# Performance work log

Hardware: AMD Instinct MI355X
Metric: run time of the kernel (lower is better)

## Reference

```python
import jax, jax.numpy as jnp
import numpy as np

# SLAYER neuron / simulation parameters (from netParams)
THETA = 10.0      # spike threshold
TAU_SR = 10.0     # synaptic (psp) alpha-kernel time constant
TAU_REF = 1.0     # refractory alpha-kernel time constant
SCALE_REF = 2.0   # refractory kernel scale
TS = 1.0          # simulation time step

N, C, H, W_SP, T = 8, 2, 50, 63, 500
OUT = 128


def _alpha_scan(x_t_first, tau, gain):
    """Causal convolution with alpha kernel k[dt] = gain*(dt*TS/tau)*exp(1-dt*TS/tau),
    k[0]=0, expressed as an exact 2-state linear recursion (O(T) instead of O(T^2)).
    x_t_first: [T, ...]. Returns [T, ...]."""
    r = jnp.exp(jnp.asarray(-TS / tau, x_t_first.dtype))
    c = jnp.asarray(gain * (TS / tau) * np.e, x_t_first.dtype)

    def step(carry, xt):
        A, B = carry          # A = sum c*dt*r^dt, B = sum c*r^dt over past inputs
        out = A               # kernel is 0 at dt=0, so x[t] does not contribute yet
        Bp = B + c * xt
        return (r * (A + Bp), r * Bp), out

    zeros = jnp.zeros_like(x_t_first[0])
    _, out = jax.lax.scan(step, (zeros, zeros), x_t_first)
    return out


def _spike_scan(u_t_first):
    """SLAYER getSpikes: sequential threshold with refractory alpha kernel
    nu[dt] = -SCALE_REF*THETA*(dt*TS/TAU_REF)*exp(1-dt*TS/TAU_REF).
    u_t_first: [T, N, O] membrane input. Returns spikes [T, N, O]."""
    r = jnp.exp(jnp.asarray(-TS / TAU_REF, u_t_first.dtype))
    c = jnp.asarray(-SCALE_REF * THETA * (TS / TAU_REF) * np.e, u_t_first.dtype)

    def step(carry, ut):
        A, B = carry
        u = ut + A                       # membrane + accumulated refractory response
        s = (u >= THETA).astype(u.dtype)
        Bp = B + c * s
        return (r * (A + Bp), r * Bp), s

    zeros = jnp.zeros_like(u_t_first[0])
    _, s = jax.lax.scan(step, (zeros, zeros), u_t_first)
    return s


def setup_inputs() -> dict:
    key = jax.random.key(0)
    k1, k2 = jax.random.split(key)
    downsampled = (jax.random.uniform(k1, (N, C, H, W_SP, T)) < 0.05).astype(jnp.float32)
    W = jax.random.normal(k2, (OUT, C * H * W_SP), dtype=jnp.float32) * 0.05
    return {"downsampled": downsampled, "W": W}


def reference(downsampled, W):
    # psp: alpha-kernel temporal filter over every input element
    x = jnp.moveaxis(downsampled, -1, 0)            # [T, N, C, H, W]
    a = _alpha_scan(x, TAU_SR, 1.0)                  # [T, N, C, H, W]
    # dense: full-spatial projection per time step
    a = a.reshape(T, N, C * H * W_SP)                # [T, N, CHW]
    u = jnp.einsum('tnc,oc->tno', a, W)              # [T, N, OUT]
    # spike generation with refractory dynamics
    s = _spike_scan(u)                               # [T, N, OUT]
    s = jnp.moveaxis(s, 0, -1)                       # [N, OUT, T]
    return s.reshape(N, OUT, 1, 1, T)                # SLAYER dense output layout
```

## Files before the change

### kernel.cpp

```cpp
#include <hip/hip_runtime.h>

#define NB 8
#define CHW 6300
#define TT 500
#define OUT 128
#define NO 1024
#define NK32 200
#define KSPLIT 8
#define NKC (NK32/KSPLIT)

typedef __attribute__((ext_vector_type(8))) _Float16 f16x8;
typedef __attribute__((ext_vector_type(4))) float f32x4;

__global__ __launch_bounds__(512) void packW(const float* __restrict__ W,
                                             _Float16* __restrict__ Wp) {
    const int tid = threadIdx.x;
    const int osub = tid >> 6;
    const int lane = tid & 63;
    const int k32 = blockIdx.x;
    const int hl = blockIdx.y;
    const int o = osub * 16 + (lane & 15);
    const int cb = k32 * 32 + (lane >> 4) * 8;

    union { _Float16 h[8]; uint4 u; } tmp;
#pragma unroll
    for (int i = 0; i < 8; i++) {
        int c = cb + i;
        float w = (c < CHW) ? W[(size_t)o * CHW + c] : 0.f;
        _Float16 hi = (_Float16)w;
        tmp.h[i] = (hl == 0) ? hi : (_Float16)((w - (float)hi) * 2048.f);
    }
    size_t lr = (((size_t)hl * NK32 + k32) * 8 + osub) * 64 + lane;
    *(uint4*)(Wp + lr * 8) = tmp.u;
}

__global__ __launch_bounds__(256, 3) void gemm(const float* __restrict__ x,
                                               const _Float16* __restrict__ Wp,
                                               float* __restrict__ vp) {
    const int L = blockIdx.x;
    const int logical = (L & 7) * 64 + (L >> 3);
    const int tb = logical & 7;
    const int n  = (logical >> 3) & 7;
    const int ks = logical >> 6;

    const int tid = threadIdx.x;
    const int wave = tid >> 6;
    const int lane = tid & 63;
    const int l15 = lane & 15;
    const int lg  = lane >> 4;
    const int k32_0 = ks * NKC;

    __shared__ _Float16 Bs[2][4][512];

    const int t_st = tb * 64 + wave * 16 + l15;
    const bool t_ok = (t_st < TT);
    const float* xrow = x + (size_t)n * CHW * TT + t_st;

    f32x4 acc[2][4][2] = {};
    f16x8 Ar0[2][2], Ar1[2][2];
    float xvA[8], xvB[8];

#define XLOAD(xv, it)                                                              \
    {                                                                              \
        const int cb_ = (k32_0 + (it)) * 32 + lg * 8;                              \
        if (((k32_0 + (it) + 1) * 32 <= CHW) && t_ok) {                            \
            _Pragma("unroll") for (int i = 0; i < 8; i++)                          \
                xv[i] = xrow[(size_t)(cb_ + i) * TT];                              \
        } else {                                                                   \
            _Pragma("unroll") for (int i = 0; i < 8; i++)                          \
                xv[i] = (t_ok && (cb_ + i) < CHW) ? xrow[(size_t)(cb_ + i) * TT]   \
                                                  : 0.f;                           \
        }                                                                          \
    }

#define XWRITE(xv, buf)                                                            \
    {                                                                              \
        union { _Float16 h[8]; uint4 u; } tw_;                                     \
        _Pragma("unroll") for (int i = 0; i < 8; i++) tw_.h[i] = (_Float16)xv[i];  \
        *(uint4*)&Bs[buf][wave][lane * 8] = tw_.u;                                 \
    }

#define ALOAD(Ar, it)                                                              \
    _Pragma("unroll") for (int of = 0; of < 2; of++)                               \
        _Pragma("unroll") for (int hl = 0; hl < 2; hl++)                           \
            Ar[of][hl] = *(const f16x8*)(Wp +                                      \
                ((((size_t)hl * NK32 + k32_0 + (it)) * 8 + wave * 2 + of) * 64 +   \
                 lane) * 8);

#define COMPUTE(buf, Ar)                                                           \
    {                                                                              \
        f16x8 bfr[4];                                                              \
        _Pragma("unroll") for (int tf = 0; tf < 4; tf++)                           \
            bfr[tf] = *(const f16x8*)&Bs[buf][tf][lane * 8];                       \
        _Pragma("unroll") for (int of = 0; of < 2; of++)                           \
            _Pragma("unroll") for (int tf = 0; tf < 4; tf++)                       \
                _Pragma("unroll") for (int hl = 0; hl < 2; hl++)                   \
                    acc[of][tf][hl] = __builtin_amdgcn_mfma_f32_16x16x32_f16(      \
                        Ar[of][hl], bfr[tf], acc[of][tf][hl], 0, 0, 0);            \
    }

    XLOAD(xvA, 0)
    XLOAD(xvB, 1)
    ALOAD(Ar0, 0)
    XWRITE(xvA, 0)
    ALOAD(Ar1, 1)
    __syncthreads();

    for (int p = 0; p < 12; ++p) {
        const int it = 2 * p;
        XLOAD(xvA, it + 2)
        COMPUTE(0, Ar0)
        XWRITE(xvB, 1)
        ALOAD(Ar0, it + 2)
        __syncthreads();
        if (p < 11) { XLOAD(xvB, it + 3) }
        COMPUTE(1, Ar1)
        XWRITE(xvA, 0)
        if (p < 11) { ALOAD(Ar1, it + 3) }
        __syncthreads();
    }
    COMPUTE(0, Ar0)

    const float inv = 1.f / 2048.f;
#pragma unroll
    for (int of = 0; of < 2; of++) {
        const int o0 = (wave * 2 + of) * 16 + lg * 4;
#pragma unroll
        for (int tf = 0; tf < 4; tf++) {
            const int t = tb * 64 + tf * 16 + l15;
            if (t < TT) {
                f32x4 vo;
#pragma unroll
                for (int r = 0; r < 4; r++)
                    vo[r] = acc[of][tf][0][r] + acc[of][tf][1][r] * inv;
                *(f32x4*)(vp + (((size_t)ks * TT + t) * NB + n) * OUT + o0) = vo;
            }
        }
    }
#undef XLOAD
#undef XWRITE
#undef ALOAD
#undef COMPUTE
}

__global__ __launch_bounds__(256) void reduceK(const float* __restrict__ vp,
                                               float* __restrict__ vred) {
    int i = blockIdx.x * 256 + threadIdx.x;
    const float4* p = (const float4*)vp;
    float4 a = p[i];
#pragma unroll
    for (int k = 1; k < KSPLIT; k++) {
        float4 b = p[(size_t)k * (TT * NO / 4) + i];
        a.x += b.x; a.y += b.y; a.z += b.z; a.w += b.w;
    }
    ((float4*)vred)[i] = a;
}

#define SCN_RA 0.9048374180359595f
#define SCN_RACA 0.24596031111569496f
#define SCN_RS 0.36787944117144233f
#define SCN_RSCS -20.0f
#define SCN_RSCS2 -40.0f
#define SCN_RSRSCS -7.3575888234288467f
#define SCN_TH 10.0f

#define CHAIN_STEP(i)                                                   \
    {                                                                   \
        float ua = Aa;                                                  \
        float w = fmaf(SCN_RS, G, ua);                                  \
        float u = sp ? (w + SCN_RSCS) : w;                              \
        bool sn = (u >= SCN_TH);                                        \
        sbuf[i][lane] = sn ? 1.f : 0.f;                                 \
        float Gb = fmaf(SCN_RS, G, H);                                  \
        G = sp ? (Gb + SCN_RSCS2) : Gb;                                 \
        float Hb = SCN_RS * H;                                          \
        H = sp ? (Hb + SCN_RSRSCS) : Hb;                                \
        sp = sn;                                                        \
        Ba = fmaf(SCN_RA, Ba, SCN_RACA * vv[i]);                        \
        Aa = fmaf(SCN_RA, Aa, Ba);                                      \
    }

__global__ __launch_bounds__(512) void scanspike(const float* __restrict__ vred,
                                                 float* __restrict__ out) {
    const int tid = threadIdx.x;
    const int wave = tid >> 6;
    const int lane = tid & 63;
    const int g0 = blockIdx.x * 64;

    __shared__ float vbuf[2][64][64];
    __shared__ float sbuf[64][65];

    for (int r = wave; r < 64; r += 8)
        vbuf[0][r][lane] = vred[(size_t)r * NO + g0 + lane];
    __syncthreads();

    float Aa = 0.f, Ba = 0.f, G = 0.f, H = 0.f;
    bool sp = false;

    for (int tb = 0; tb < 8; ++tb) {
        const int cur = tb & 1;
        const int t0 = tb * 64;
        const int cnt = (tb == 7) ? 52 : 64;

        if (wave == 0) {
            if (cnt == 64) {
                float vv[64];
#pragma unroll
                for (int i = 0; i < 64; ++i) vv[i] = vbuf[cur][i][lane];
#pragma unroll
                for (int i = 0; i < 64; ++i) CHAIN_STEP(i)
            } else {
                float vv[52];
#pragma unroll
                for (int i = 0; i < 52; ++i) vv[i] = vbuf[cur][i][lane];
#pragma unroll
                for (int i = 0; i < 52; ++i) CHAIN_STEP(i)
            }
        } else if (tb < 7) {
            const int nt0 = t0 + 64;
            const int ncnt = (tb == 6) ? 52 : 64;
            for (int r = wave - 1; r < ncnt; r += 7)
                vbuf[cur ^ 1][r][lane] = vred[(size_t)(nt0 + r) * NO + g0 + lane];
        }
        __syncthreads();

#pragma unroll
        for (int j = 0; j < 8; ++j) {
            int r = wave * 8 + j;
            int gr = g0 + r;
            int nn = gr >> 7;
            int oo = gr & 127;
            if (lane < cnt)
                out[((size_t)nn * OUT + oo) * TT + t0 + lane] = sbuf[lane][r];
        }
        __syncthreads();
    }
}

extern "C" void kernel_launch(void* const* d_in, const int* in_sizes, int n_in,
                              void* d_out, int out_size, void* d_ws, size_t ws_size,
                              hipStream_t stream) {
    const float* x = (const float*)d_in[0];
    const float* W = (const float*)d_in[1];
    float* out = (float*)d_out;

    _Float16* Wp   = (_Float16*)d_ws;
    float*    vp   = (float*)((char*)d_ws + 3276800);
    float*    vred = (float*)((char*)d_ws + 3276800 + 16384000);

    packW<<<dim3(NK32, 2), 512, 0, stream>>>(W, Wp);
    gemm<<<512, 256, 0, stream>>>(x, Wp, vp);
    reduceK<<<TT * NO / 4 / 256, 256, 0, stream>>>(vp, vred);
    scanspike<<<16, 512, 0, stream>>>(vred, out);
}
```

Before: 60.60 us.

## Deepen global x prefetch to three register buffers in GEMM main loop

The GEMM main loop now rotates three register buffers for the strided x loads instead of two, so each global load is issued two stages before it is written to shared memory. The loop is unrolled six-way and the W fragment loads are rescheduled to one stage ahead. This aims to hide global-memory latency better. The extra registers force launch bounds down from 3 to 2 blocks per SM, which lowers occupancy.

After: 58.58 us. 1.03x faster.

```diff
diff --git a/kernel.cpp b/kernel.cpp
--- a/kernel.cpp
+++ b/kernel.cpp
@@ -34,7 +34,7 @@
     *(uint4*)(Wp + lr * 8) = tmp.u;
 }
 
-__global__ __launch_bounds__(256, 3) void gemm(const float* __restrict__ x,
+__global__ __launch_bounds__(256, 2) void gemm(const float* __restrict__ x,
                                                const _Float16* __restrict__ Wp,
                                                float* __restrict__ vp) {
     const int L = blockIdx.x;
@@ -58,7 +58,7 @@
 
     f32x4 acc[2][4][2] = {};
     f16x8 Ar0[2][2], Ar1[2][2];
-    float xvA[8], xvB[8];
+    float xvA[8], xvB[8], xvC[8];
 
 #define XLOAD(xv, it)                                                              \
     {                                                                              \
@@ -101,22 +101,42 @@
 
     XLOAD(xvA, 0)
     XLOAD(xvB, 1)
+    XLOAD(xvC, 2)
     ALOAD(Ar0, 0)
     XWRITE(xvA, 0)
-    ALOAD(Ar1, 1)
     __syncthreads();
 
-    for (int p = 0; p < 12; ++p) {
-        const int it = 2 * p;
-        XLOAD(xvA, it + 2)
+    for (int q = 0; q < 4; ++q) {
+        const int it0 = 6 * q;
+        if (it0 + 3 <= 24) { XLOAD(xvA, it0 + 3) }
         COMPUTE(0, Ar0)
         XWRITE(xvB, 1)
-        ALOAD(Ar0, it + 2)
-        __syncthreads();
-        if (p < 11) { XLOAD(xvB, it + 3) }
+        ALOAD(Ar1, it0 + 1)
+        __syncthreads();
+        if (it0 + 4 <= 24) { XLOAD(xvB, it0 + 4) }
+        COMPUTE(1, Ar1)
+        XWRITE(xvC, 0)
+        ALOAD(Ar0, it0 + 2)
+        __syncthreads();
+        if (it0 + 5 <= 24) { XLOAD(xvC, it0 + 5) }
+        COMPUTE(0, Ar0)
+        XWRITE(xvA, 1)
+        ALOAD(Ar1, it0 + 3)
+        __syncthreads();
+        if (it0 + 6 <= 24) { XLOAD(xvA, it0 + 6) }
+        COMPUTE(1, Ar1)
+        XWRITE(xvB, 0)
+        ALOAD(Ar0, it0 + 4)
+        __syncthreads();
+        if (it0 + 7 <= 24) { XLOAD(xvB, it0 + 7) }
+        COMPUTE(0, Ar0)
+        XWRITE(xvC, 1)
+        ALOAD(Ar1, it0 + 5)
+        __syncthreads();
+        if (it0 + 8 <= 24) { XLOAD(xvC, it0 + 8) }
         COMPUTE(1, Ar1)
         XWRITE(xvA, 0)
-        if (p < 11) { ALOAD(Ar1, it + 3) }
+        ALOAD(Ar0, it0 + 6)
         __syncthreads();
     }
     COMPUTE(0, Ar0)
```

## Load x with float4 along time and transpose through LDS staging buffer

Applied to the files above, without the earlier changes.

Replaces the per-thread scalar strided loads of x (eight channels at stride TT) with float4 loads that are contiguous along time. The loaded tiles are staged in a padded fp32 LDS buffer and transposed into the f16 B-fragment layout. The goal is wider, better-coalesced global reads of the large input, paid for with extra LDS traffic, a deeper software pipeline and more registers. To make room, the occupancy hint drops from 3 to 2 blocks per CU.

After: 58.37 us. 1.04x faster.

```diff
diff --git a/kernel.cpp b/kernel.cpp
--- a/kernel.cpp
+++ b/kernel.cpp
@@ -34,7 +34,7 @@
     *(uint4*)(Wp + lr * 8) = tmp.u;
 }
 
-__global__ __launch_bounds__(256, 3) void gemm(const float* __restrict__ x,
+__global__ __launch_bounds__(256, 2) void gemm(const float* __restrict__ x,
                                                const _Float16* __restrict__ Wp,
                                                float* __restrict__ vp) {
     const int L = blockIdx.x;
@@ -48,36 +48,52 @@
     const int lane = tid & 63;
     const int l15 = lane & 15;
     const int lg  = lane >> 4;
+    const int rr  = lg;
+    const int ch  = l15;
     const int k32_0 = ks * NKC;
 
+    __shared__ float    Ls[2][32][65];
     __shared__ _Float16 Bs[2][4][512];
 
-    const int t_st = tb * 64 + wave * 16 + l15;
-    const bool t_ok = (t_st < TT);
-    const float* xrow = x + (size_t)n * CHW * TT + t_st;
+    const float* xn = x + (size_t)n * CHW * TT;
+    const int toff = tb * 64 + ch * 4;
+    const bool tbok = (tb < 7);
 
     f32x4 acc[2][4][2] = {};
     f16x8 Ar0[2][2], Ar1[2][2];
-    float xvA[8], xvB[8];
-
-#define XLOAD(xv, it)                                                              \
-    {                                                                              \
-        const int cb_ = (k32_0 + (it)) * 32 + lg * 8;                              \
-        if (((k32_0 + (it) + 1) * 32 <= CHW) && t_ok) {                            \
-            _Pragma("unroll") for (int i = 0; i < 8; i++)                          \
-                xv[i] = xrow[(size_t)(cb_ + i) * TT];                              \
-        } else {                                                                   \
-            _Pragma("unroll") for (int i = 0; i < 8; i++)                          \
-                xv[i] = (t_ok && (cb_ + i) < CHW) ? xrow[(size_t)(cb_ + i) * TT]   \
-                                                  : 0.f;                           \
+    float4 sA[2], sB[2];
+    const float4 f4z = make_float4(0.f, 0.f, 0.f, 0.f);
+
+#define XG(set, it)                                                                \
+    {                                                                              \
+        _Pragma("unroll") for (int p = 0; p < 2; p++) {                            \
+            const int r_ = wave * 8 + p * 4 + rr;                                  \
+            const int c_ = (k32_0 + (it)) * 32 + r_;                               \
+            const bool v_ = (c_ < CHW) && (tbok || ch < 13);                       \
+            set[p] = v_ ? *(const float4*)(xn + (size_t)c_ * TT + toff) : f4z;     \
         }                                                                          \
     }
 
-#define XWRITE(xv, buf)                                                            \
-    {                                                                              \
-        union { _Float16 h[8]; uint4 u; } tw_;                                     \
-        _Pragma("unroll") for (int i = 0; i < 8; i++) tw_.h[i] = (_Float16)xv[i];  \
-        *(uint4*)&Bs[buf][wave][lane * 8] = tw_.u;                                 \
+#define DSW(set, bufL)                                                             \
+    {                                                                              \
+        _Pragma("unroll") for (int p = 0; p < 2; p++) {                            \
+            const int r_ = wave * 8 + p * 4 + rr;                                  \
+            Ls[bufL][r_][ch * 4 + 0] = set[p].x;                                   \
+            Ls[bufL][r_][ch * 4 + 1] = set[p].y;                                   \
+            Ls[bufL][r_][ch * 4 + 2] = set[p].z;                                   \
+            Ls[bufL][r_][ch * 4 + 3] = set[p].w;                                   \
+        }                                                                          \
+    }
+
+#define TRANS(bufL, bufB)                                                          \
+    {                                                                              \
+        float tv_[8];                                                              \
+        _Pragma("unroll") for (int i = 0; i < 8; i++)                              \
+            tv_[i] = Ls[bufL][lg * 8 + i][wave * 16 + l15];                        \
+        union { _Float16 h[8]; uint4 u; } tc_;                                     \
+        _Pragma("unroll") for (int i = 0; i < 8; i++)                              \
+            tc_.h[i] = (_Float16)tv_[i];                                           \
+        *(uint4*)&Bs[bufB][wave][lane * 8] = tc_.u;                                \
     }
 
 #define ALOAD(Ar, it)                                                              \
@@ -99,24 +115,30 @@
                         Ar[of][hl], bfr[tf], acc[of][tf][hl], 0, 0, 0);            \
     }
 
-    XLOAD(xvA, 0)
-    XLOAD(xvB, 1)
+    XG(sA, 0)
+    XG(sB, 1)
+    DSW(sA, 0)
+    XG(sA, 2)
+    __syncthreads();
+    TRANS(0, 0)
+    DSW(sB, 1)
+    XG(sB, 3)
     ALOAD(Ar0, 0)
-    XWRITE(xvA, 0)
-    ALOAD(Ar1, 1)
     __syncthreads();
 
     for (int p = 0; p < 12; ++p) {
         const int it = 2 * p;
-        XLOAD(xvA, it + 2)
+        ALOAD(Ar1, it + 1)
+        DSW(sA, 0)
+        if (p <= 10) { XG(sA, it + 4) }
+        TRANS(1, 1)
         COMPUTE(0, Ar0)
-        XWRITE(xvB, 1)
+        __syncthreads();
         ALOAD(Ar0, it + 2)
-        __syncthreads();
-        if (p < 11) { XLOAD(xvB, it + 3) }
+        if (p <= 10) { DSW(sB, 1) }
+        if (p <= 9)  { XG(sB, it + 5) }
+        TRANS(0, 0)
         COMPUTE(1, Ar1)
-        XWRITE(xvA, 0)
-        if (p < 11) { ALOAD(Ar1, it + 3) }
         __syncthreads();
     }
     COMPUTE(0, Ar0)
@@ -137,8 +159,9 @@
             }
         }
     }
-#undef XLOAD
-#undef XWRITE
+#undef XG
+#undef DSW
+#undef TRANS
 #undef ALOAD
 #undef COMPUTE
 }
```
